# Performance work log

Measured on AMD Instinct MI355X. Metric: run time of the kernel, lower is better.

The kernel has to match this reference:

```python
import jax, jax.numpy as jnp
import numpy as np

D = 192

def layer_norm(x, g, b, eps=1e-5):
    m = jnp.mean(x, -1, keepdims=True)
    v = jnp.var(x, -1, keepdims=True)
    return (x - m) * jax.lax.rsqrt(v + eps) * g + b

def _bilinear(v, x, y, H, W):
    # v: (N, nH, H*W, hd); x, y: (N, nH, Q) fractional pixel coords (grid_sample, align_corners=False, zero pad)
    x0 = jnp.floor(x); y0 = jnp.floor(y)
    wx = x - x0; wy = y - y0
    x0i = x0.astype(jnp.int32); y0i = y0.astype(jnp.int32)
    def gather(xi, yi):
        valid = (xi >= 0) & (xi < W) & (yi >= 0) & (yi < H)
        idx = jnp.clip(yi, 0, H - 1) * W + jnp.clip(xi, 0, W - 1)
        g = jnp.take_along_axis(v, idx[..., None], axis=2)
        return jnp.where(valid[..., None], g, 0.0)
    return (gather(x0i, y0i) * ((1 - wx) * (1 - wy))[..., None]
            + gather(x0i + 1, y0i) * (wx * (1 - wy))[..., None]
            + gather(x0i, y0i + 1) * ((1 - wx) * wy)[..., None]
            + gather(x0i + 1, y0i + 1) * (wx * wy)[..., None])

def _linear1d(v, p, T):
    # v: (N, nH, T, hd); p: (N, nH, Q) fractional temporal coords
    p0 = jnp.floor(p); wp = p - p0; p0i = p0.astype(jnp.int32)
    def gather(pi):
        valid = (pi >= 0) & (pi < T)
        idx = jnp.clip(pi, 0, T - 1)
        g = jnp.take_along_axis(v, idx[..., None], axis=2)
        return jnp.where(valid[..., None], g, 0.0)
    return gather(p0i) * (1 - wp)[..., None] + gather(p0i + 1) * wp[..., None]

def msdeform_2d(q, ref, H, W, nH, P, off_w, off_b, aw_w, aw_b, v_w, v_b, o_w, o_b):
    # single-level MSDeformAttn; q == input_flatten (self-attn style usage)
    N, L, d = q.shape; hd = d // nH
    v = (q @ v_w + v_b).reshape(N, L, nH, hd).transpose(0, 2, 1, 3)  # (N,nH,L,hd)
    off = (q @ off_w + off_b).reshape(N, L, nH, P, 2)
    aw = jax.nn.softmax((q @ aw_w + aw_b).reshape(N, L, nH, P), axis=-1)
    norm = jnp.array([W, H], dtype=q.dtype)
    loc = ref[:, :, None, :, :] + off / norm  # (N,L,nH,P,2)
    x = (loc[..., 0] * W - 0.5).transpose(0, 2, 1, 3).reshape(N, nH, L * P)
    y = (loc[..., 1] * H - 0.5).transpose(0, 2, 1, 3).reshape(N, nH, L * P)
    samp = _bilinear(v, x, y, H, W).reshape(N, nH, L, P, hd)
    out = jnp.einsum('nlhp,nhlpd->nlhd', aw, samp).reshape(N, L, d)
    return out @ o_w + o_b

def msdeform_1d(q, ref, T, nH, P, off_w, off_b, aw_w, aw_b, v_w, v_b, o_w, o_b):
    N, L, d = q.shape; hd = d // nH  # L == T
    v = (q @ v_w + v_b).reshape(N, L, nH, hd).transpose(0, 2, 1, 3)
    off = (q @ off_w + off_b).reshape(N, L, nH, P)
    aw = jax.nn.softmax((q @ aw_w + aw_b).reshape(N, L, nH, P), axis=-1)
    loc = ref[:, :, 0, 0][:, :, None, None] + off / T  # (N,L,nH,P)
    p = (loc * T - 0.5).transpose(0, 2, 1, 3).reshape(N, nH, L * P)
    samp = _linear1d(v, p, T).reshape(N, nH, L, P, hd)
    out = jnp.einsum('nlhp,nhlpd->nlhd', aw, samp).reshape(N, L, d)
    return out @ o_w + o_b

def setup_inputs():
    key = jax.random.key(0)
    ks = jax.random.split(key, 24)
    d = D; n, t, h, w = 2, 8, 48, 48
    f = lambda k, shape, s=0.05: jax.random.normal(k, shape, dtype=jnp.float32) * s
    return {
        'x': jax.random.normal(ks[0], (n, d, t, h, w), dtype=jnp.float32),
        'fuse': jax.random.normal(ks[1], (n, d, h, w), dtype=jnp.float32),
        'conv_w': f(ks[2], (d, 2 * d)), 'conv_b': f(ks[3], (d,)),
        's_off_w': f(ks[4], (d, 16 * 2 * 2), 0.01), 's_off_b': f(ks[5], (16 * 2 * 2,), 0.01),
        's_aw_w': f(ks[6], (d, 16 * 2)), 's_aw_b': f(ks[7], (16 * 2,)),
        's_v_w': f(ks[8], (d, d)), 's_v_b': f(ks[9], (d,)),
        's_o_w': f(ks[10], (d, d)), 's_o_b': f(ks[11], (d,)),
        't_off_w': f(ks[12], (d, 8 * 4), 0.01), 't_off_b': f(ks[13], (8 * 4,), 0.01),
        't_aw_w': f(ks[14], (d, 8 * 4)), 't_aw_b': f(ks[15], (8 * 4,)),
        't_v_w': f(ks[16], (d, d)), 't_v_b': f(ks[17], (d,)),
        't_o_w': f(ks[18], (d, d)), 't_o_b': f(ks[19], (d,)),
        'ln1_g': jnp.ones((d,), jnp.float32), 'ln1_b': jnp.zeros((d,), jnp.float32),
        'ln2_g': jnp.ones((d,), jnp.float32), 'ln2_b': jnp.zeros((d,), jnp.float32),
        'ln3_g': jnp.ones((d,), jnp.float32), 'ln3_b': jnp.zeros((d,), jnp.float32),
        'lin1_w': f(ks[20], (2 * d, d)), 'lin1_b': f(ks[21], (d,)),
        'lin2_w': f(ks[22], (d, d)), 'lin2_b': f(ks[23], (d,)),
    }

def reference(x, fuse, conv_w, conv_b, s_off_w, s_off_b, s_aw_w, s_aw_b, s_v_w, s_v_b, s_o_w, s_o_b,
              t_off_w, t_off_b, t_aw_w, t_aw_b, t_v_w, t_v_b, t_o_w, t_o_b,
              ln1_g, ln1_b, ln2_g, ln2_b, ln3_g, ln3_b, lin1_w, lin1_b, lin2_w, lin2_b):
    n, c, t, h, w = x.shape; d = c
    fuse_e = jnp.broadcast_to(fuse[:, :, None, :, :], (n, c, t, h, w))
    xc = jnp.concatenate([x, fuse_e], axis=1)                      # (n,2c,t,h,w)
    xm = jnp.einsum('ncthw,oc->nothw', xc, conv_w) + conv_b[None, :, None, None, None]
    # spatial deformable attention over h*w tokens per (n*t)
    x_space = xm.transpose(0, 2, 3, 4, 1).reshape(n * t, h * w, d)
    yy, xx = jnp.meshgrid(jnp.linspace(0, 1, h, dtype=x.dtype), jnp.linspace(0, 1, w, dtype=x.dtype), indexing='ij')
    ref2 = jnp.broadcast_to(jnp.stack([yy, xx], -1).reshape(1, h * w, 1, 2), (n * t, h * w, 1, 2))
    s_out = msdeform_2d(x_space, ref2, h, w, 16, 2, s_off_w, s_off_b, s_aw_w, s_aw_b, s_v_w, s_v_b, s_o_w, s_o_b)
    # temporal deformable attention over t tokens per (n*h*w)
    x_temp = xm.transpose(0, 3, 4, 1, 2).reshape(n * h * w, t, d)
    ref1 = jnp.broadcast_to(jnp.linspace(0, 1, t, dtype=x.dtype).reshape(1, t, 1, 1), (n * h * w, t, 1, 1))
    t_out = msdeform_1d(x_temp, ref1, t, 8, 4, t_off_w, t_off_b, t_aw_w, t_aw_b, t_v_w, t_v_b, t_o_w, t_o_b)
    # residual + LN, then the original's raw .view(h*w, t, n, c) reinterpretation (replicated faithfully)
    xs = layer_norm(x_space + s_out, ln1_g, ln1_b)
    xs = xs.reshape(h * w, t, n, d).transpose(1, 0, 2, 3).reshape(t * h * w, n, d)
    xt = layer_norm(x_temp + t_out, ln2_g, ln2_b)
    xt = xt.reshape(h * w, t, n, d).transpose(1, 0, 2, 3).reshape(t * h * w, n, d)
    x_st = jnp.concatenate([xt, xs], axis=-1)                      # (t*h*w, n, 2d)
    x_st = jax.nn.gelu(x_st @ lin1_w + lin1_b, approximate=False) @ lin2_w + lin2_b
    x_st = x_st.reshape(t, h, w, n, d).transpose(3, 4, 0, 1, 2)    # (n,d,t,h,w)
    xm = xm + x_st
    out = layer_norm(xm.transpose(0, 2, 3, 4, 1), ln3_g, ln3_b).transpose(0, 4, 1, 2, 3)
    return out
```

## Files before the change

kernel.cpp:

```cpp
#include <hip/hip_runtime.h>
#include <hip/hip_bf16.h>
#include <math.h>

typedef __hip_bfloat16 bf16;
typedef __attribute__((ext_vector_type(8))) short bf16x8;
typedef __attribute__((ext_vector_type(4))) float f32x4;

#define N_    2
#define D_    192
#define T_    8
#define H_    48
#define W_    48
#define HW_   2304
#define NPOS  36864
#define BUF_ELEMS 7077888

#define OFF_SOFFW 0
#define OFF_SOFFB 12288
#define OFF_SAWW  12352
#define OFF_SAWB  18496
#define OFF_SVW   18528
#define OFF_SVB   55392
#define OFF_SOW   55584
#define OFF_SOB   92448
#define OFF_TOFFW 92640
#define OFF_TOFFB 98784
#define OFF_TAWW  98816
#define OFF_TAWB  104960
#define OFF_TVW   104992
#define OFF_TVB   141856
#define OFF_TOW   142048
#define OFF_TOB   178912
#define OFF_LN1G  179104
#define OFF_LN1B  179296
#define OFF_LN2G  179488
#define OFF_LN2B  179680
#define OFF_LN3G  179872
#define OFF_LN3B  180064
#define OFF_LIN1W 180256
#define OFF_LIN1B 253984
#define OFF_LIN2W 254176
#define OFF_LIN2B 291040
#define OFF_CONVB 291232
#define WF_TOTAL  291424

#define PB_SCOMB 0
#define PB_SOW   55296
#define PB_TCOMB 92160
#define PB_TOW   141312
#define PB_LIN1  178176
#define PB_CONV  251904
#define PB_LIN2  325632
#define PB_TOTAL 362496

static __device__ __forceinline__ float b2f(bf16 v){ return __bfloat162float(v); }
static __device__ __forceinline__ bf16  f2b(float v){ return __float2bfloat16(v); }
static __device__ __forceinline__ float lo16(unsigned u){
  unsigned v = u<<16; return *(float*)&v;
}
static __device__ __forceinline__ float hi16(unsigned u){
  unsigned v = u & 0xFFFF0000u; return *(float*)&v;
}
static __device__ __forceinline__ unsigned pk2(float a, float b){
  bf16 x = f2b(a), y = f2b(b);
  return (unsigned)*(unsigned short*)&x | ((unsigned)*(unsigned short*)&y << 16);
}
static __device__ __forceinline__ int detect_bf(const void* ln1g){
  unsigned u = *(const unsigned*)ln1g;
  return __builtin_amdgcn_readfirstlane(((u & 0xFFFFu) != 0u) ? 1 : 0);
}
static __device__ __forceinline__ int swz8(int ch, int r){ return ch ^ (r & 7); }

struct KPtrs { const void* p[27]; };
static __device__ const int WSZ[27] = {12288,64,6144,32,36864,192,36864,192,
  6144,32,6144,32,36864,192,36864,192, 192,192,192,192,192,192, 73728,192,36864,192, 192};

__global__ void k_cvtw(KPtrs P, float* __restrict__ WF, const void* __restrict__ ln1g){
  int bf = detect_bf(ln1g);
  int gid = blockIdx.x*256 + threadIdx.x;
  if (gid >= WF_TOTAL) return;
  int e = 0, off = 0;
  while (gid >= off + WSZ[e]){ off += WSZ[e]; ++e; }
  int i = gid - off;
  WF[gid] = bf ? b2f(((const bf16*)P.p[e])[i]) : ((const float*)P.p[e])[i];
}

__global__ void k_wt(const void* __restrict__ W, float* __restrict__ Wt, const void* __restrict__ ln1g){
  int bf = detect_bf(ln1g);
  int i = blockIdx.x*256 + threadIdx.x;
  if (i < 384*192){
    int c = i/192, o = i%192;
    Wt[i] = bf ? b2f(((const bf16*)W)[o*384+c]) : ((const float*)W)[o*384+c];
  }
}

__global__ void k_packB(const float* __restrict__ WF, const float* __restrict__ Wt,
                        bf16* __restrict__ PB){
  const int NB[7]  = {108,72,96,72,144,144,72};
  const int NT[7]  = {18,12,16,12,12,12,12};
  const int DST[7] = {PB_SCOMB, PB_SOW, PB_TCOMB, PB_TOW, PB_LIN1, PB_CONV, PB_LIN2};
  int bid = blockIdx.x, e = 0, start = 0;
  while (e < 6 && bid >= start + NB[e]){ start += NB[e]; ++e; }
  int local = bid - start;
  int nt = local % NT[e], kt = local / NT[e];
  int l = threadIdx.x;
  int k0 = kt*32 + (l>>4)*8, n0 = nt*16 + (l&15);
  bf16* D = PB + DST[e] + ((long)(kt*NT[e]+nt)*64 + l)*8;
  #pragma unroll
  for (int i=0;i<8;++i){
    int k = k0 + i;
    float v;
    if (e==0){
      if (n0<192)      v = WF[OFF_SVW  + k*192 + n0];
      else if (n0<256) v = WF[OFF_SOFFW+ k*64  + (n0-192)];
      else             v = WF[OFF_SAWW + k*32  + (n0-256)];
    } else if (e==1)   v = WF[OFF_SOW  + k*192 + n0];
    else if (e==2){
      if (n0<192)      v = WF[OFF_TVW  + k*192 + n0];
      else if (n0<224) v = WF[OFF_TOFFW+ k*32  + (n0-192)];
      else             v = WF[OFF_TAWW + k*32  + (n0-224)];
    } else if (e==3)   v = WF[OFF_TOW  + k*192 + n0];
    else if (e==4)     v = WF[OFF_LIN1W+ k*192 + n0];
    else if (e==5)     v = Wt[k*192 + n0];
    else               v = WF[OFF_LIN2W+ k*192 + n0];
    D[i] = f2b(v);
  }
}

template<int KTOT, int MODE, int CF32>
__global__ void __launch_bounds__(256) k_gemm(const bf16* __restrict__ A0, const bf16* __restrict__ A1,
      const bf16* __restrict__ Bp, const float* __restrict__ bias, void* __restrict__ C_){
  __shared__ bf16 sA[64*KTOT];
  const int NCH = KTOT/8;
  int tid = threadIdx.x;
  int r0 = blockIdx.x*64;
  for (int i=tid; i<64*NCH; i+=256){
    int r = i/NCH, ch = i - r*NCH;
    int grow;
    if (MODE==1){
      int q = r0+r, f = q>>1, n2 = q&1;
      int t2 = f/HW_, hw2 = f - t2*HW_;
      grow = hw2*16 + t2*2 + n2;
    } else grow = r0+r;
    const bf16* src = (MODE==1 && ch>=24) ? (A1 + (long)grow*192 + (ch-24)*8)
                                          : (A0 + (long)grow*192 + ch*8);
    *(bf16x8*)(sA + r*KTOT + swz8(ch,r)*8) = *(const bf16x8*)src;
  }
  __syncthreads();
  int wid = tid>>6, lane = tid&63;
  int m16 = lane&15, kg = lane>>4;
  f32x4 acc[4][3];
  #pragma unroll
  for (int mi=0;mi<4;++mi)
    #pragma unroll
    for (int ni=0;ni<3;++ni) acc[mi][ni] = (f32x4){0.f,0.f,0.f,0.f};

  const int NKT = KTOT/32;
  for (int kt=0; kt<NKT; ++kt){
    bf16x8 b[3];
    #pragma unroll
    for (int ni=0;ni<3;++ni){
      int nt = wid*3 + ni;
      b[ni] = *(const bf16x8*)(Bp + ((long)(kt*12+nt)*64 + lane)*8);
    }
    bf16x8 a[4];
    #pragma unroll
    for (int mi=0;mi<4;++mi){
      int row = mi*16 + m16;
      a[mi] = *(const bf16x8*)(sA + row*KTOT + swz8(kt*4+kg,row)*8);
    }
    #pragma unroll
    for (int mi=0;mi<4;++mi)
      #pragma unroll
      for (int ni=0;ni<3;++ni)
        acc[mi][ni] = __builtin_amdgcn_mfma_f32_16x16x32_bf16(a[mi], b[ni], acc[mi][ni], 0,0,0);
  }
  const float IS2 = 0.70710678118654752f;
  #pragma unroll
  for (int mi=0;mi<4;++mi)
    #pragma unroll
    for (int ni=0;ni<3;++ni){
      int col = (wid*3+ni)*16 + m16;
      float bv = bias[col];
      #pragma unroll
      for (int rg=0;rg<4;++rg){
        int row = r0 + mi*16 + kg*4 + rg;
        float v = acc[mi][ni][rg] + bv;
        if (MODE==1) v = 0.5f*v*(1.f+erff(v*IS2));
        if (CF32) ((float*)C_)[(long)row*192 + col] = v;
        else      ((bf16*)C_)[(long)row*192 + col] = f2b(v);
      }
    }
}

template<int NWAVES, int NTW, int NO>
__global__ void __launch_bounds__(NWAVES*64) k_gemmC(const float* __restrict__ A,
      const bf16* __restrict__ Bp, const float* __restrict__ biasV,
      const float* __restrict__ biasO, const float* __restrict__ biasA,
      bf16* __restrict__ Cv, float* __restrict__ Coa){
  __shared__ bf16 sA[64*192];
  const int NT_TOT = NWAVES*NTW;
  const int NOA = NT_TOT*16 - 192;
  int tid = threadIdx.x;
  int r0 = blockIdx.x*64;
  for (int i=tid; i<64*48; i+=NWAVES*64){
    int r = i/48, c4 = i - r*48;
    float4 v = *(const float4*)(A + (long)(r0+r)*192 + c4*4);
    bf16* dst = sA + r*192 + swz8(c4>>1, r)*8 + (c4&1)*4;
    dst[0]=f2b(v.x); dst[1]=f2b(v.y); dst[2]=f2b(v.z); dst[3]=f2b(v.w);
  }
  __syncthreads();
  int wid = tid>>6, lane = tid&63;
  int m16 = lane&15, kg = lane>>4;
  f32x4 acc[4][NTW];
  #pragma unroll
  for (int mi=0;mi<4;++mi)
    #pragma unroll
    for (int ni=0;ni<NTW;++ni) acc[mi][ni] = (f32x4){0.f,0.f,0.f,0.f};
  for (int kt=0; kt<6; ++kt){
    bf16x8 b[NTW];
    #pragma unroll
    for (int ni=0;ni<NTW;++ni){
      int nt = wid*NTW + ni;
      b[ni] = *(const bf16x8*)(Bp + ((long)(kt*NT_TOT+nt)*64 + lane)*8);
    }
    bf16x8 a[4];
    #pragma unroll
    for (int mi=0;mi<4;++mi){
      int row = mi*16 + m16;
      a[mi] = *(const bf16x8*)(sA + row*192 + swz8(kt*4+kg,row)*8);
    }
    #pragma unroll
    for (int mi=0;mi<4;++mi)
      #pragma unroll
      for (int ni=0;ni<NTW;++ni)
        acc[mi][ni] = __builtin_amdgcn_mfma_f32_16x16x32_bf16(a[mi], b[ni], acc[mi][ni], 0,0,0);
  }
  #pragma unroll
  for (int mi=0;mi<4;++mi)
    #pragma unroll
    for (int ni=0;ni<NTW;++ni){
      int col = (wid*NTW+ni)*16 + m16;
      #pragma unroll
      for (int rg=0;rg<4;++rg){
        int row = r0 + mi*16 + kg*4 + rg;
        float v = acc[mi][ni][rg];
        if (col < 192)           Cv[(long)row*192 + col] = f2b(v + biasV[col]);
        else if (col < 192+NO)   Coa[(long)row*NOA + (col-192)] = v + biasO[col-192];
        else                     Coa[(long)row*NOA + (col-192)] = v + biasA[col-192-NO];
      }
    }
}

__global__ void __launch_bounds__(256) k_convm(const void* __restrict__ x, const void* __restrict__ fuse,
      const bf16* __restrict__ Bp, const float* __restrict__ bias, float* __restrict__ B0,
      const void* __restrict__ ln1g){
  __shared__ bf16 sA[64*384];
  int bf = detect_bf(ln1g);
  int bid = blockIdx.x;
  int n = bid/(8*36), rm = bid%(8*36);
  int t = rm/36, hb = rm%36;
  int hw0 = hb*64;
  int tid = threadIdx.x;
  if (bf){
    for (int i=tid; i<384*64; i+=256){
      int c = i>>6, j = i&63;
      long idx = (c<192) ? ((long)((n*192+c)*8 + t)*HW_ + hw0 + j)
                         : ((long)(n*192+(c-192))*HW_ + hw0 + j);
      bf16 v = ((const bf16*)((c<192)?x:fuse))[idx];
      sA[j*384 + swz8(c>>3, j)*8 + (c&7)] = v;
    }
  } else {
    for (int i=tid; i<384*64; i+=256){
      int c = i>>6, j = i&63;
      long idx = (c<192) ? ((long)((n*192+c)*8 + t)*HW_ + hw0 + j)
                         : ((long)(n*192+(c-192))*HW_ + hw0 + j);
      float v = ((const float*)((c<192)?x:fuse))[idx];
      sA[j*384 + swz8(c>>3, j)*8 + (c&7)] = f2b(v);
    }
  }
  __syncthreads();
  int wid = tid>>6, lane = tid&63;
  int m16 = lane&15, kg = lane>>4;
  f32x4 acc[4][3];
  #pragma unroll
  for (int mi=0;mi<4;++mi)
    #pragma unroll
    for (int ni=0;ni<3;++ni) acc[mi][ni] = (f32x4){0.f,0.f,0.f,0.f};
  for (int kt=0; kt<12; ++kt){
    bf16x8 b[3];
    #pragma unroll
    for (int ni=0;ni<3;++ni){
      int nt = wid*3 + ni;
      b[ni] = *(const bf16x8*)(Bp + ((long)(kt*12+nt)*64 + lane)*8);
    }
    bf16x8 a[4];
    #pragma unroll
    for (int mi=0;mi<4;++mi){
      int row = mi*16 + m16;
      a[mi] = *(const bf16x8*)(&sA[row*384 + swz8(kt*4+kg,row)*8]);
    }
    #pragma unroll
    for (int mi=0;mi<4;++mi)
      #pragma unroll
      for (int ni=0;ni<3;++ni)
        acc[mi][ni] = __builtin_amdgcn_mfma_f32_16x16x32_bf16(a[mi], b[ni], acc[mi][ni], 0,0,0);
  }
  long posbase = (long)(n*8+t)*HW_ + hw0;
  #pragma unroll
  for (int mi=0;mi<4;++mi)
    #pragma unroll
    for (int ni=0;ni<3;++ni){
      int col = (wid*3+ni)*16 + m16;
      float bv = bias[col];
      #pragma unroll
      for (int rg=0;rg<4;++rg){
        int row = mi*16 + kg*4 + rg;
        B0[(posbase + row)*192 + col] = acc[mi][ni][rg] + bv;
      }
    }
}

__global__ void __launch_bounds__(256) k_xt(const float* __restrict__ S0, float* __restrict__ S4){
  __shared__ float s[8*1536];
  int b0 = blockIdx.x*8, tid = threadIdx.x;
  for (int i=tid; i<8*1536; i+=256){
    int j = i/1536, rest = i - j*1536;
    int t = rest/192, o = rest - t*192;
    int b = b0 + j;
    int n = b/HW_, hw = b - n*HW_;
    s[j*1536 + (o/24)*192 + (o%24)*8 + t] = S0[((long)((n*8+t)*HW_) + hw)*192 + o];
  }
  __syncthreads();
  for (int i=tid; i<8*1536; i+=256){
    int j = i/1536, rest = i - j*1536;
    S4[(long)(b0+j)*1536 + rest] = s[j*1536 + rest];
  }
}

__global__ void __launch_bounds__(256) k_sfuse(const float* __restrict__ OA, const bf16* __restrict__ V,
    const bf16* __restrict__ Bp, const float* __restrict__ biasO,
    const float* __restrict__ X, const float* __restrict__ g, const float* __restrict__ bta,
    bf16* __restrict__ outXS){
  __shared__ char smem[32768 + 12288];
  __shared__ float mrs[32][2];
  float (*tup)[8] = (float(*)[8])smem;
  float (*yb)[193] = (float(*)[193])smem;
  bf16* sA = (bf16*)(smem + 32768);
  int r0 = blockIdx.x*32, tid = threadIdx.x;
  int nt = r0 / HW_;
  for (int i=tid; i<512; i+=256){
    int row = i>>4, head = i&15;
    int l = (r0+row) % HW_;
    int iy = l/48, jx = l%48;
    const float* oa = OA + (long)(r0+row)*96;
    float l0 = oa[64+head*2], l1 = oa[64+head*2+1];
    float m = fmaxf(l0,l1);
    float e0 = __expf(l0-m), e1 = __expf(l1-m);
    float inv = 1.f/(e0+e1);
    const float SC = 48.0f/47.0f;
    #pragma unroll
    for (int p=0;p<2;++p){
      float aw = (p==0?e0:e1)*inv;
      float fx = iy*SC + oa[head*4+p*2+0] - 0.5f;
      float fy = jx*SC + oa[head*4+p*2+1] - 0.5f;
      float x0f = floorf(fx), y0f = floorf(fy);
      float wx = fx-x0f, wy = fy-y0f;
      int x0 = (int)x0f, y0 = (int)y0f;
      int x1 = x0+1, y1 = y0+1;
      bool vx0 = (x0>=0 && x0<48), vx1 = (x1>=0 && x1<48);
      bool vy0 = (y0>=0 && y0<48), vy1 = (y1>=0 && y1<48);
      int cx0 = min(max(x0,0),47), cx1 = min(max(x1,0),47);
      int cy0 = min(max(y0,0),47), cy1 = min(max(y1,0),47);
      float* tp = tup[row*32 + head*2 + p];
      tp[0] = (vx0&&vy0) ? aw*(1.f-wx)*(1.f-wy) : 0.f;
      tp[1] = (vx1&&vy0) ? aw*wx*(1.f-wy)       : 0.f;
      tp[2] = (vx0&&vy1) ? aw*(1.f-wx)*wy       : 0.f;
      tp[3] = (vx1&&vy1) ? aw*wx*wy             : 0.f;
      tp[4] = (float)(cy0*48+cx0);
      tp[5] = (float)(cy0*48+cx1);
      tp[6] = (float)(cy1*48+cx0);
      tp[7] = (float)(cy1*48+cx1);
    }
  }
  __syncthreads();
  const unsigned* vbu = (const unsigned*)(V + (long)nt*HW_*192);
  for (int it=tid; it<3072; it+=256){
    int row = it/96, cp = it - row*96;
    int head = cp/6;
    float a0 = 0.f, a1 = 0.f;
    #pragma unroll
    for (int p=0;p<2;++p){
      const float* tp = tup[row*32 + head*2 + p];
      #pragma unroll
      for (int c=0;c<4;++c){
        float w = tp[c];
        int idx = (int)tp[4+c];
        unsigned u = vbu[idx*96 + cp];
        a0 += w*lo16(u);
        a1 += w*hi16(u);
      }
    }
    *(unsigned*)(sA + row*192 + swz8(cp>>2,row)*8 + (cp&3)*2) = pk2(a0,a1);
  }
  __syncthreads();
  int wid = tid>>6, lane = tid&63;
  int m16 = lane&15, kg = lane>>4;
  f32x4 acc[2][3];
  #pragma unroll
  for (int mi=0;mi<2;++mi)
    #pragma unroll
    for (int ni=0;ni<3;++ni) acc[mi][ni] = (f32x4){0.f,0.f,0.f,0.f};
  for (int kt=0; kt<6; ++kt){
    bf16x8 b[3];
    #pragma unroll
    for (int ni=0;ni<3;++ni){
      int ntb = wid*3 + ni;
      b[ni] = *(const bf16x8*)(Bp + ((long)(kt*12+ntb)*64 + lane)*8);
    }
    bf16x8 a[2];
    #pragma unroll
    for (int mi=0;mi<2;++mi){
      int row = mi*16 + m16;
      a[mi] = *(const bf16x8*)(sA + row*192 + swz8(kt*4+kg,row)*8);
    }
    #pragma unroll
    for (int mi=0;mi<2;++mi)
      #pragma unroll
      for (int ni=0;ni<3;++ni)
        acc[mi][ni] = __builtin_amdgcn_mfma_f32_16x16x32_bf16(a[mi], b[ni], acc[mi][ni], 0,0,0);
  }
  __syncthreads();
  #pragma unroll
  for (int mi=0;mi<2;++mi)
    #pragma unroll
    for (int ni=0;ni<3;++ni){
      int col = (wid*3+ni)*16 + m16;
      float bv = biasO[col];
      #pragma unroll
      for (int rg=0;rg<4;++rg){
        int lr = mi*16 + kg*4 + rg;
        yb[lr][col] = acc[mi][ni][rg] + bv + X[(long)(r0+lr)*192 + col];
      }
    }
  __syncthreads();
  for (int rr=0; rr<8; ++rr){
    int row = wid*8 + rr;
    float s=0.f, s2=0.f;
    #pragma unroll
    for (int e=0;e<3;++e){
      float v = yb[row][lane*3+e];
      s += v; s2 += v*v;
    }
    #pragma unroll
    for (int off=32; off>0; off>>=1){ s += __shfl_xor(s,off); s2 += __shfl_xor(s2,off); }
    if (lane==0){
      float mean = s*(1.f/192.f);
      mrs[row][0] = mean;
      mrs[row][1] = rsqrtf(s2*(1.f/192.f) - mean*mean + 1e-5f);
    }
  }
  __syncthreads();
  for (int i=tid; i<3072; i+=256){
    int row = i/96, cp = i - row*96;
    float mean = mrs[row][0], rstd = mrs[row][1];
    int c0 = cp*2, c1 = c0+1;
    float v0 = (yb[row][c0]-mean)*rstd*g[c0] + bta[c0];
    float v1 = (yb[row][c1]-mean)*rstd*g[c1] + bta[c1];
    ((unsigned*)outXS)[(long)(r0+row)*96 + cp] = pk2(v0,v1);
  }
}

__global__ void __launch_bounds__(256) k_tfuse(const float* __restrict__ OT, const bf16* __restrict__ V,
    const bf16* __restrict__ Bp, const float* __restrict__ biasO,
    const float* __restrict__ X, const float* __restrict__ g, const float* __restrict__ bta,
    bf16* __restrict__ outXT){
  __shared__ char smem[24704 + 12288];
  __shared__ unsigned sV[3072];
  __shared__ float mrs[32][2];
  float (*tup)[4] = (float(*)[4])smem;
  float (*yb)[193] = (float(*)[193])smem;
  bf16* sA = (bf16*)(smem + 24704);
  int r0 = blockIdx.x*32, tid = threadIdx.x;
  int b0 = r0 >> 3;
  {
    int row = tid>>3, head = tid&7;
    int tau = (r0+row) & 7;
    float pref = tau*(8.0f/7.0f) - 0.5f;
    const float* ot = OT + (long)(r0+row)*64;
    float l0=ot[32+head*4], l1=ot[32+head*4+1], l2=ot[32+head*4+2], l3=ot[32+head*4+3];
    float m = fmaxf(fmaxf(l0,l1), fmaxf(l2,l3));
    float e0=__expf(l0-m), e1=__expf(l1-m), e2=__expf(l2-m), e3=__expf(l3-m);
    float inv = 1.f/(e0+e1+e2+e3);
    float ee[4] = {e0,e1,e2,e3};
    #pragma unroll
    for (int p=0;p<4;++p){
      float aw = ee[p]*inv;
      float fp = pref + ot[head*4+p];
      float p0f = floorf(fp);
      float wp = fp - p0f;
      int p0 = (int)p0f, p1 = p0+1;
      float* tp = tup[row*32 + head*4 + p];
      tp[0] = (p0>=0 && p0<8) ? aw*(1.f-wp) : 0.f;
      tp[1] = (p1>=0 && p1<8) ? aw*wp       : 0.f;
      tp[2] = (float)min(max(p0,0),7);
      tp[3] = (float)min(max(p1,0),7);
    }
  }
  {
    const unsigned* Vu = (const unsigned*)(V + (long)b0*1536);
    for (int i=tid; i<3072; i+=256) sV[i] = Vu[i];
  }
  __syncthreads();
  for (int it=tid; it<3072; it+=256){
    int row = it/96, cp = it - row*96;
    int head = cp/12;
    const unsigned* vb = sV + (row>>3)*768;
    float a0 = 0.f, a1 = 0.f;
    #pragma unroll
    for (int p=0;p<4;++p){
      const float* tp = tup[row*32 + head*4 + p];
      unsigned u0 = vb[(int)tp[2]*96 + cp];
      unsigned u1 = vb[(int)tp[3]*96 + cp];
      a0 += tp[0]*lo16(u0) + tp[1]*lo16(u1);
      a1 += tp[0]*hi16(u0) + tp[1]*hi16(u1);
    }
    *(unsigned*)(sA + row*192 + swz8(cp>>2,row)*8 + (cp&3)*2) = pk2(a0,a1);
  }
  __syncthreads();
  int wid = tid>>6, lane = tid&63;
  int m16 = lane&15, kg = lane>>4;
  f32x4 acc[2][3];
  #pragma unroll
  for (int mi=0;mi<2;++mi)
    #pragma unroll
    for (int ni=0;ni<3;++ni) acc[mi][ni] = (f32x4){0.f,0.f,0.f,0.f};
  for (int kt=0; kt<6; ++kt){
    bf16x8 b[3];
    #pragma unroll
    for (int ni=0;ni<3;++ni){
      int ntb = wid*3 + ni;
      b[ni] = *(const bf16x8*)(Bp + ((long)(kt*12+ntb)*64 + lane)*8);
    }
    bf16x8 a[2];
    #pragma unroll
    for (int mi=0;mi<2;++mi){
      int row = mi*16 + m16;
      a[mi] = *(const bf16x8*)(sA + row*192 + swz8(kt*4+kg,row)*8);
    }
    #pragma unroll
    for (int mi=0;mi<2;++mi)
      #pragma unroll
      for (int ni=0;ni<3;++ni)
        acc[mi][ni] = __builtin_amdgcn_mfma_f32_16x16x32_bf16(a[mi], b[ni], acc[mi][ni], 0,0,0);
  }
  __syncthreads();
  #pragma unroll
  for (int mi=0;mi<2;++mi)
    #pragma unroll
    for (int ni=0;ni<3;++ni){
      int col = (wid*3+ni)*16 + m16;
      float bv = biasO[col];
      #pragma unroll
      for (int rg=0;rg<4;++rg){
        int lr = mi*16 + kg*4 + rg;
        yb[lr][col] = acc[mi][ni][rg] + bv + X[(long)(r0+lr)*192 + col];
      }
    }
  __syncthreads();
  for (int rr=0; rr<8; ++rr){
    int row = wid*8 + rr;
    float s=0.f, s2=0.f;
    #pragma unroll
    for (int e=0;e<3;++e){
      float v = yb[row][lane*3+e];
      s += v; s2 += v*v;
    }
    #pragma unroll
    for (int off=32; off>0; off>>=1){ s += __shfl_xor(s,off); s2 += __shfl_xor(s2,off); }
    if (lane==0){
      float mean = s*(1.f/192.f);
      mrs[row][0] = mean;
      mrs[row][1] = rsqrtf(s2*(1.f/192.f) - mean*mean + 1e-5f);
    }
  }
  __syncthreads();
  for (int i=tid; i<3072; i+=256){
    int row = i/96, cp = i - row*96;
    float mean = mrs[row][0], rstd = mrs[row][1];
    int c0 = cp*2, c1 = c0+1;
    float v0 = (yb[row][c0]-mean)*rstd*g[c0] + bta[c0];
    float v1 = (yb[row][c1]-mean)*rstd*g[c1] + bta[c1];
    ((unsigned*)outXT)[(long)(r0+row)*96 + cp] = pk2(v0,v1);
  }
}

__global__ void __launch_bounds__(256) k_final3(const float* __restrict__ B0, const bf16* __restrict__ hid,
    const bf16* __restrict__ Bp, const float* __restrict__ bias2,
    const float* __restrict__ g, const float* __restrict__ bta,
    void* __restrict__ out, const void* __restrict__ ln1g){
  __shared__ float yb[32][193];
  __shared__ float mrs[32][2];
  bf16* sA = (bf16*)&yb[0][0];
  int bf = detect_bf(ln1g);
  int pos0 = blockIdx.x*32;
  int tid = threadIdx.x, wid = tid>>6, lane = tid&63;
  int m16 = lane&15, kg = lane>>4;
  int n2 = pos0/(T_*HW_), rem0 = pos0%(T_*HW_);
  long qrow0 = (long)rem0*2 + n2;
  for (int i=tid; i<32*24; i+=256){
    int r = i/24, ch = i - r*24;
    *(bf16x8*)(sA + r*192 + swz8(ch,r)*8) =
        *(const bf16x8*)(hid + (qrow0 + r*2)*192 + ch*8);
  }
  __syncthreads();
  f32x4 acc[2][3];
  #pragma unroll
  for (int mi=0;mi<2;++mi)
    #pragma unroll
    for (int ni=0;ni<3;++ni) acc[mi][ni] = (f32x4){0.f,0.f,0.f,0.f};
  for (int kt=0; kt<6; ++kt){
    bf16x8 b[3];
    #pragma unroll
    for (int ni=0;ni<3;++ni){
      int nt = wid*3 + ni;
      b[ni] = *(const bf16x8*)(Bp + ((long)(kt*12+nt)*64 + lane)*8);
    }
    bf16x8 a[2];
    #pragma unroll
    for (int mi=0;mi<2;++mi){
      int row = mi*16 + m16;
      a[mi] = *(const bf16x8*)(sA + row*192 + swz8(kt*4+kg,row)*8);
    }
    #pragma unroll
    for (int mi=0;mi<2;++mi)
      #pragma unroll
      for (int ni=0;ni<3;++ni)
        acc[mi][ni] = __builtin_amdgcn_mfma_f32_16x16x32_bf16(a[mi], b[ni], acc[mi][ni], 0,0,0);
  }
  __syncthreads();
  #pragma unroll
  for (int mi=0;mi<2;++mi)
    #pragma unroll
    for (int ni=0;ni<3;++ni){
      int col = (wid*3+ni)*16 + m16;
      float bv = bias2[col];
      #pragma unroll
      for (int rg=0;rg<4;++rg){
        int lr = mi*16 + kg*4 + rg;
        yb[lr][col] = acc[mi][ni][rg] + bv + B0[(long)(pos0+lr)*192 + col];
      }
    }
  __syncthreads();
  for (int rr=0; rr<8; ++rr){
    int row = wid*8 + rr;
    float s=0.f, s2=0.f;
    #pragma unroll
    for (int e=0;e<3;++e){
      float v = yb[row][lane*3+e];
      s += v; s2 += v*v;
    }
    #pragma unroll
    for (int off=32; off>0; off>>=1){ s += __shfl_xor(s,off); s2 += __shfl_xor(s2,off); }
    if (lane==0){
      float mean = s*(1.f/192.f);
      mrs[row][0] = mean;
      mrs[row][1] = rsqrtf(s2*(1.f/192.f) - mean*mean + 1e-5f);
    }
  }
  __syncthreads();
  int t2 = rem0/HW_, hw0 = rem0%HW_;
  int j = lane & 31;
  float mean = mrs[j][0], rstd = mrs[j][1];
  for (int cc=0; cc<48; cc+=2){
    int c = wid*48 + cc + (lane>>5);
    float val = (yb[j][c]-mean)*rstd*g[c] + bta[c];
    long idx = ((long)(n2*192 + c)*8 + t2)*HW_ + hw0 + j;
    if (bf) ((bf16*)out)[idx] = f2b(val);
    else    ((float*)out)[idx] = val;
  }
}

extern "C" void kernel_launch(void* const* d_in, const int* in_sizes, int n_in,
                              void* d_out, int out_size, void* d_ws, size_t ws_size,
                              hipStream_t stream){
  const void* x      = d_in[0];
  const void* fuse   = d_in[1];
  const void* conv_w = d_in[2];
  const void* ln1g_raw = d_in[20];

  float* S0f = (float*)d_ws;
  float* S4f = S0f + BUF_ELEMS;
  float* WS2 = S4f + BUF_ELEMS;
  bf16*  Vb  = (bf16*)WS2;
  float* OA  = WS2 + BUF_ELEMS/2;
  bf16*  HID = (bf16*)WS2;
  float* WS4 = WS2 + BUF_ELEMS;
  bf16*  XS  = (bf16*)WS4;
  float* WS5 = WS4 + BUF_ELEMS/2;
  bf16*  XT  = (bf16*)WS5;
  float* WF  = WS5 + BUF_ELEMS/2;
  float* Wt  = WF + WF_TOTAL;
  bf16*  PB  = (bf16*)(Wt + 384*192);

  KPtrs P;
  for (int i=0;i<26;++i) P.p[i] = d_in[4+i];
  P.p[26] = d_in[3];

  k_cvtw <<<(WF_TOTAL+255)/256, 256, 0, stream>>>(P, WF, ln1g_raw);
  k_wt   <<<288, 256, 0, stream>>>(conv_w, Wt, ln1g_raw);
  k_packB<<<708, 64, 0, stream>>>(WF, Wt, PB);

  k_convm<<<576, 256, 0, stream>>>(x, fuse, PB+PB_CONV, WF+OFF_CONVB, S0f, ln1g_raw);
  k_xt   <<<576, 256, 0, stream>>>(S0f, S4f);

  k_gemmC<6,3,64><<<576, 384, 0, stream>>>(S0f, PB+PB_SCOMB, WF+OFF_SVB, WF+OFF_SOFFB, WF+OFF_SAWB, Vb, OA);
  k_sfuse<<<NPOS/32, 256, 0, stream>>>(OA, Vb, PB+PB_SOW, WF+OFF_SOB, S0f,
                                       WF+OFF_LN1G, WF+OFF_LN1B, XS);

  k_gemmC<4,4,32><<<576, 256, 0, stream>>>(S4f, PB+PB_TCOMB, WF+OFF_TVB, WF+OFF_TOFFB, WF+OFF_TAWB, Vb, OA);
  k_tfuse<<<NPOS/32, 256, 0, stream>>>(OA, Vb, PB+PB_TOW, WF+OFF_TOB, S4f,
                                       WF+OFF_LN2G, WF+OFF_LN2B, XT);

  k_gemm<384,1,0><<<576, 256, 0, stream>>>(XT, XS, PB+PB_LIN1, WF+OFF_LIN1B, HID);
  k_final3<<<NPOS/32, 256, 0, stream>>>(S0f, HID, PB+PB_LIN2, WF+OFF_LIN2B,
                                        WF+OFF_LN3G, WF+OFF_LN3B, d_out, ln1g_raw);
}
```

Measured before the change: 218.9 us.

## Fuse temporal transpose, projection GEMM and deformable attention into one kernel

Replaces the separate transpose kernel (k_xt), the temporal combined-projection GEMM and k_tfuse with a single k_tpath kernel. It reads S0 directly, builds the transposed tile in shared memory as bf16, and runs the value/offset/weight GEMM and the sampling and output GEMM on chip. The residual is reloaded from S0 into shared memory. This removes the S4 buffer, the Vb/OA round trips through global memory and two launches, at the cost of recomputing the transposed residual read and a heavier kernel with more shared memory per block.

Measured after the change: 195.4 us. 1.12x faster.

```diff
diff --git a/kernel.cpp b/kernel.cpp
--- a/kernel.cpp
+++ b/kernel.cpp
@@ -321,23 +321,6 @@
     }
 }
 
-__global__ void __launch_bounds__(256) k_xt(const float* __restrict__ S0, float* __restrict__ S4){
-  __shared__ float s[8*1536];
-  int b0 = blockIdx.x*8, tid = threadIdx.x;
-  for (int i=tid; i<8*1536; i+=256){
-    int j = i/1536, rest = i - j*1536;
-    int t = rest/192, o = rest - t*192;
-    int b = b0 + j;
-    int n = b/HW_, hw = b - n*HW_;
-    s[j*1536 + (o/24)*192 + (o%24)*8 + t] = S0[((long)((n*8+t)*HW_) + hw)*192 + o];
-  }
-  __syncthreads();
-  for (int i=tid; i<8*1536; i+=256){
-    int j = i/1536, rest = i - j*1536;
-    S4[(long)(b0+j)*1536 + rest] = s[j*1536 + rest];
-  }
-}
-
 __global__ void __launch_bounds__(256) k_sfuse(const float* __restrict__ OA, const bf16* __restrict__ V,
     const bf16* __restrict__ Bp, const float* __restrict__ biasO,
     const float* __restrict__ X, const float* __restrict__ g, const float* __restrict__ bta,
@@ -471,23 +454,87 @@
   }
 }
 
-__global__ void __launch_bounds__(256) k_tfuse(const float* __restrict__ OT, const bf16* __restrict__ V,
-    const bf16* __restrict__ Bp, const float* __restrict__ biasO,
-    const float* __restrict__ X, const float* __restrict__ g, const float* __restrict__ bta,
+__global__ void __launch_bounds__(256) k_tpath(const float* __restrict__ S0,
+    const bf16* __restrict__ BpC, const float* __restrict__ biasV,
+    const float* __restrict__ biasOf, const float* __restrict__ biasAw,
+    const bf16* __restrict__ BpO, const float* __restrict__ biasO,
+    const float* __restrict__ g, const float* __restrict__ bta,
     bf16* __restrict__ outXT){
-  __shared__ char smem[24704 + 12288];
-  __shared__ unsigned sV[3072];
+  __shared__ char smem[49152];
   __shared__ float mrs[32][2];
-  float (*tup)[4] = (float(*)[4])smem;
-  float (*yb)[193] = (float(*)[193])smem;
-  bf16* sA = (bf16*)(smem + 24704);
-  int r0 = blockIdx.x*32, tid = threadIdx.x;
-  int b0 = r0 >> 3;
+  bf16*     sV   = (bf16*)smem;
+  float*    slog = (float*)(smem + 12288);
+  bf16*     sST  = (bf16*)(smem + 20480);
+  float (*tup)[4] = (float(*)[4])(smem + 32768);
+  float (*yb)[193] = (float(*)[193])(smem + 20480);
+  int bid = blockIdx.x, tid = threadIdx.x;
+  int b0 = bid*4, r0 = bid*32;
+  int n = b0 / HW_, hw0 = b0 - n*HW_;
+  int wid = tid>>6, lane = tid&63;
+  int m16 = lane&15, kg = lane>>4;
+
+  for (int i=tid; i<1536; i+=256){
+    int j = i/384, rem = i - j*384;
+    int t = rem/48, c4 = rem - t*48;
+    float4 v = *(const float4*)(S0 + ((long)((n*8+t)*HW_) + hw0+j)*192 + c4*4);
+    int o0 = c4*4;
+    int tau = o0/24;
+    int lrow = j*8 + tau;
+    bf16* base = sST + lrow*192;
+    #pragma unroll
+    for (int e=0;e<4;++e){
+      int ch = (o0+e)%24;
+      base[swz8(ch,lrow)*8 + t] = f2b(((const float*)&v)[e]);
+    }
+  }
+  __syncthreads();
+  {
+    f32x4 acc[2][4];
+    #pragma unroll
+    for (int mi=0;mi<2;++mi)
+      #pragma unroll
+      for (int ni=0;ni<4;++ni) acc[mi][ni] = (f32x4){0.f,0.f,0.f,0.f};
+    for (int kt=0; kt<6; ++kt){
+      bf16x8 b[4];
+      #pragma unroll
+      for (int ni=0;ni<4;++ni){
+        int ntb = wid*4 + ni;
+        b[ni] = *(const bf16x8*)(BpC + ((long)(kt*16+ntb)*64 + lane)*8);
+      }
+      bf16x8 a[2];
+      #pragma unroll
+      for (int mi=0;mi<2;++mi){
+        int row = mi*16 + m16;
+        a[mi] = *(const bf16x8*)(sST + row*192 + swz8(kt*4+kg,row)*8);
+      }
+      #pragma unroll
+      for (int mi=0;mi<2;++mi)
+        #pragma unroll
+        for (int ni=0;ni<4;++ni)
+          acc[mi][ni] = __builtin_amdgcn_mfma_f32_16x16x32_bf16(a[mi], b[ni], acc[mi][ni], 0,0,0);
+    }
+    __syncthreads();
+    #pragma unroll
+    for (int mi=0;mi<2;++mi)
+      #pragma unroll
+      for (int ni=0;ni<4;++ni){
+        int col = (wid*4+ni)*16 + m16;
+        #pragma unroll
+        for (int rg=0;rg<4;++rg){
+          int lr = mi*16 + kg*4 + rg;
+          float v = acc[mi][ni][rg];
+          if (col < 192)      sV[lr*192 + col] = f2b(v + biasV[col]);
+          else if (col < 224) slog[lr*64 + (col-192)] = v + biasOf[col-192];
+          else                slog[lr*64 + (col-192)] = v + biasAw[col-224];
+        }
+      }
+  }
+  __syncthreads();
   {
     int row = tid>>3, head = tid&7;
-    int tau = (r0+row) & 7;
+    int tau = row & 7;
     float pref = tau*(8.0f/7.0f) - 0.5f;
-    const float* ot = OT + (long)(r0+row)*64;
+    const float* ot = slog + row*64;
     float l0=ot[32+head*4], l1=ot[32+head*4+1], l2=ot[32+head*4+2], l3=ot[32+head*4+3];
     float m = fmaxf(fmaxf(l0,l1), fmaxf(l2,l3));
     float e0=__expf(l0-m), e1=__expf(l1-m), e2=__expf(l2-m), e3=__expf(l3-m);
@@ -507,52 +554,63 @@
       tp[3] = (float)min(max(p1,0),7);
     }
   }
+  __syncthreads();
   {
-    const unsigned* Vu = (const unsigned*)(V + (long)b0*1536);
-    for (int i=tid; i<3072; i+=256) sV[i] = Vu[i];
-  }
-  __syncthreads();
-  for (int it=tid; it<3072; it+=256){
-    int row = it/96, cp = it - row*96;
-    int head = cp/12;
-    const unsigned* vb = sV + (row>>3)*768;
-    float a0 = 0.f, a1 = 0.f;
-    #pragma unroll
-    for (int p=0;p<4;++p){
-      const float* tp = tup[row*32 + head*4 + p];
-      unsigned u0 = vb[(int)tp[2]*96 + cp];
-      unsigned u1 = vb[(int)tp[3]*96 + cp];
-      a0 += tp[0]*lo16(u0) + tp[1]*lo16(u1);
-      a1 += tp[0]*hi16(u0) + tp[1]*hi16(u1);
-    }
-    *(unsigned*)(sA + row*192 + swz8(cp>>2,row)*8 + (cp&3)*2) = pk2(a0,a1);
-  }
-  __syncthreads();
-  int wid = tid>>6, lane = tid&63;
-  int m16 = lane&15, kg = lane>>4;
-  f32x4 acc[2][3];
+    const unsigned* sVu = (const unsigned*)sV;
+    for (int it=tid; it<3072; it+=256){
+      int row = it/96, cp = it - row*96;
+      int head = cp/12;
+      const unsigned* vb = sVu + (row>>3)*8*96;
+      float a0 = 0.f, a1 = 0.f;
+      #pragma unroll
+      for (int p=0;p<4;++p){
+        const float* tp = tup[row*32 + head*4 + p];
+        unsigned u0 = vb[(int)tp[2]*96 + cp];
+        unsigned u1 = vb[(int)tp[3]*96 + cp];
+        a0 += tp[0]*lo16(u0) + tp[1]*lo16(u1);
+        a1 += tp[0]*hi16(u0) + tp[1]*hi16(u1);
+      }
+      *(unsigned*)(sST + row*192 + swz8(cp>>2,row)*8 + (cp&3)*2) = pk2(a0,a1);
+    }
+  }
+  __syncthreads();
+  f32x4 acc2[2][3];
   #pragma unroll
   for (int mi=0;mi<2;++mi)
     #pragma unroll
-    for (int ni=0;ni<3;++ni) acc[mi][ni] = (f32x4){0.f,0.f,0.f,0.f};
+    for (int ni=0;ni<3;++ni) acc2[mi][ni] = (f32x4){0.f,0.f,0.f,0.f};
   for (int kt=0; kt<6; ++kt){
     bf16x8 b[3];
     #pragma unroll
     for (int ni=0;ni<3;++ni){
       int ntb = wid*3 + ni;
-      b[ni] = *(const bf16x8*)(Bp + ((long)(kt*12+ntb)*64 + lane)*8);
+      b[ni] = *(const bf16x8*)(BpO + ((long)(kt*12+ntb)*64 + lane)*8);
     }
     bf16x8 a[2];
     #pragma unroll
     for (int mi=0;mi<2;++mi){
       int row = mi*16 + m16;
-      a[mi] = *(const bf16x8*)(sA + row*192 + swz8(kt*4+kg,row)*8);
+      a[mi] = *(const bf16x8*)(sST + row*192 + swz8(kt*4+kg,row)*8);
     }
     #pragma unroll
     for (int mi=0;mi<2;++mi)
       #pragma unroll
       for (int ni=0;ni<3;++ni)
-        acc[mi][ni] = __builtin_amdgcn_mfma_f32_16x16x32_bf16(a[mi], b[ni], acc[mi][ni], 0,0,0);
+        acc2[mi][ni] = __builtin_amdgcn_mfma_f32_16x16x32_bf16(a[mi], b[ni], acc2[mi][ni], 0,0,0);
+  }
+  __syncthreads();
+  for (int i=tid; i<1536; i+=256){
+    int j = i/384, rem = i - j*384;
+    int t = rem/48, c4 = rem - t*48;
+    float4 v = *(const float4*)(S0 + ((long)((n*8+t)*HW_) + hw0+j)*192 + c4*4);
+    int o0 = c4*4;
+    int tau = o0/24;
+    int lrow = j*8 + tau;
+    #pragma unroll
+    for (int e=0;e<4;++e){
+      int k = ((o0+e)%24)*8 + t;
+      yb[lrow][k] = ((const float*)&v)[e];
+    }
   }
   __syncthreads();
   #pragma unroll
@@ -564,7 +622,7 @@
       #pragma unroll
       for (int rg=0;rg<4;++rg){
         int lr = mi*16 + kg*4 + rg;
-        yb[lr][col] = acc[mi][ni][rg] + bv + X[(long)(r0+lr)*192 + col];
+        yb[lr][col] += acc2[mi][ni][rg] + bv;
       }
     }
   __syncthreads();
@@ -690,8 +748,7 @@
   const void* ln1g_raw = d_in[20];
 
   float* S0f = (float*)d_ws;
-  float* S4f = S0f + BUF_ELEMS;
-  float* WS2 = S4f + BUF_ELEMS;
+  float* WS2 = S0f + BUF_ELEMS;
   bf16*  Vb  = (bf16*)WS2;
   float* OA  = WS2 + BUF_ELEMS/2;
   bf16*  HID = (bf16*)WS2;
@@ -712,15 +769,13 @@
   k_packB<<<708, 64, 0, stream>>>(WF, Wt, PB);
 
   k_convm<<<576, 256, 0, stream>>>(x, fuse, PB+PB_CONV, WF+OFF_CONVB, S0f, ln1g_raw);
-  k_xt   <<<576, 256, 0, stream>>>(S0f, S4f);
 
   k_gemmC<6,3,64><<<576, 384, 0, stream>>>(S0f, PB+PB_SCOMB, WF+OFF_SVB, WF+OFF_SOFFB, WF+OFF_SAWB, Vb, OA);
   k_sfuse<<<NPOS/32, 256, 0, stream>>>(OA, Vb, PB+PB_SOW, WF+OFF_SOB, S0f,
                                        WF+OFF_LN1G, WF+OFF_LN1B, XS);
 
-  k_gemmC<4,4,32><<<576, 256, 0, stream>>>(S4f, PB+PB_TCOMB, WF+OFF_TVB, WF+OFF_TOFFB, WF+OFF_TAWB, Vb, OA);
-  k_tfuse<<<NPOS/32, 256, 0, stream>>>(OA, Vb, PB+PB_TOW, WF+OFF_TOB, S4f,
-                                       WF+OFF_LN2G, WF+OFF_LN2B, XT);
+  k_tpath<<<NPOS/32, 256, 0, stream>>>(S0f, PB+PB_TCOMB, WF+OFF_TVB, WF+OFF_TOFFB, WF+OFF_TAWB,
+                                       PB+PB_TOW, WF+OFF_TOB, WF+OFF_LN2G, WF+OFF_LN2B, XT);
 
   k_gemm<384,1,0><<<576, 256, 0, stream>>>(XT, XS, PB+PB_LIN1, WF+OFF_LIN1B, HID);
   k_final3<<<NPOS/32, 256, 0, stream>>>(S0f, HID, PB+PB_LIN2, WF+OFF_LIN2B,
```
